# Performance work log

Hardware: AMD Instinct MI355X
Metric: run time of the kernel (lower is better)

The kernel has to match this reference:

```python
import jax, jax.numpy as jnp
import numpy as np

B, T, DIM, HEADS, KPROJ = 4, 4096, 1024, 16, 256
DH = DIM // HEADS  # dim_head = 64


def setup_inputs() -> dict:
    key = jax.random.key(0)
    k1, k2, k3, k4 = jax.random.split(key, 4)
    x = jax.random.normal(k1, (B, T, DIM), dtype=jnp.float32)
    proj_mat = jax.random.normal(k2, (T, KPROJ), dtype=jnp.float32)
    # to_qvk: Linear(dim, 3*dim, bias=False); store as [dim, 3*dim] so y = x @ Wqkv
    Wqkv = jax.random.normal(k3, (DIM, 3 * DIM), dtype=jnp.float32) / np.sqrt(DIM)
    # W_0: Linear(dim, dim, bias=False); stored as [dim, dim] so y = x @ W0
    W0 = jax.random.normal(k4, (DIM, DIM), dtype=jnp.float32) / np.sqrt(DIM)
    return {"x": x, "proj_mat": proj_mat, "Wqkv": Wqkv, "W0": W0}


def reference(x, proj_mat, Wqkv, W0):
    scale = DH ** (-0.5)
    qkv = jnp.einsum('btc,cf->btf', x, Wqkv)  # [B,T,3*dim]
    # einops 'b t (d k h) -> k b h t d' with k=3, h=HEADS: last axis splits as (d, 3, h)
    qkv = qkv.reshape(B, T, DH, 3, HEADS)
    qkv = jnp.transpose(qkv, (3, 0, 4, 1, 2))  # [3, B, H, T, DH]
    q, k, v = qkv[0], qkv[1], qkv[2]
    # Linformer low-rank projection of k and v along sequence axis
    k = jnp.einsum('bhjd,jk->bhkd', k, proj_mat)  # [B,H,KPROJ,DH]
    v = jnp.einsum('bhjd,jk->bhkd', v, proj_mat)
    # scaled dot-product attention
    scores = jnp.einsum('bhid,bhjd->bhij', q, k) * scale  # [B,H,T,KPROJ]
    attn = jax.nn.softmax(scores, axis=-1)
    out = jnp.einsum('bhij,bhjd->bhid', attn, v)  # [B,H,T,DH]
    out = jnp.transpose(out, (0, 2, 1, 3)).reshape(B, T, HEADS * DH)
    return jnp.einsum('btc,cf->btf', out, W0)
```

## Files before the change

kernel.cpp:

```cpp
#include <hip/hip_runtime.h>
#include <stdint.h>
#include <stddef.h>

#define TB    4096
#define NDIM  1024
#define NH    16
#define KPROJ 256
#define DH    64
#define NBH   64

typedef _Float16 f16;
typedef _Float16 f16x8 __attribute__((ext_vector_type(8)));
typedef float    f32x4 __attribute__((ext_vector_type(4)));

__device__ __forceinline__ void glds16(const f16* g, f16* l) {
  __builtin_amdgcn_global_load_lds((const __attribute__((address_space(1))) void*)g,
                                   (__attribute__((address_space(3))) void*)l, 16, 0, 0);
}

__launch_bounds__(256)
__global__ void cvt_x(const float* __restrict__ in, f16* __restrict__ out) {
  size_t i = ((size_t)blockIdx.x * 256 + threadIdx.x) * 8;
  float4 v0 = *(const float4*)(in + i);
  float4 v1 = *(const float4*)(in + i + 4);
  union { f16 h[8]; uint4 u; } pk;
  pk.h[0] = (f16)v0.x; pk.h[1] = (f16)v0.y; pk.h[2] = (f16)v0.z; pk.h[3] = (f16)v0.w;
  pk.h[4] = (f16)v1.x; pk.h[5] = (f16)v1.y; pk.h[6] = (f16)v1.z; pk.h[7] = (f16)v1.w;
  *(uint4*)(out + i) = pk.u;
}

__launch_bounds__(256)
__global__ void cvt_t(const float* __restrict__ in, f16* __restrict__ out, int R, int C) {
  __shared__ __align__(16) f16 s[64][72];
  const int tid = threadIdx.x;
  const int c0 = blockIdx.x * 64, r0 = blockIdx.y * 64;
#pragma unroll
  for (int it = 0; it < 4; ++it) {
    int chunk = it * 256 + tid;
    int r_l = chunk >> 4, c4 = (chunk & 15) * 4;
    float4 v = *(const float4*)(in + (size_t)(r0 + r_l) * C + c0 + c4);
    s[c4 + 0][r_l] = (f16)v.x; s[c4 + 1][r_l] = (f16)v.y;
    s[c4 + 2][r_l] = (f16)v.z; s[c4 + 3][r_l] = (f16)v.w;
  }
  __syncthreads();
#pragma unroll
  for (int it = 0; it < 2; ++it) {
    int chunk = it * 256 + tid;
    int c_l = chunk >> 3, rc = (chunk & 7) * 8;
    *(uint4*)(out + (size_t)(c0 + c_l) * R + r0 + rc) = *(const uint4*)&s[c_l][rc];
  }
}

__launch_bounds__(256)
__global__ void k_q(const f16* __restrict__ Xh, const f16* __restrict__ Wt,
                    f16* __restrict__ qt) {
  __shared__ __align__(16) f16 As[128 * 32];
  __shared__ __align__(16) f16 Bs[128 * 32];
  const int tid = threadIdx.x;
  const int w = tid >> 6, lane = tid & 63;
  const int quad = lane >> 4, l15 = lane & 15;
  const int bn0 = blockIdx.x * 128, bm0 = blockIdx.y * 128;
  const int wm = (w & 1) * 64, wn = (w >> 1) * 64;
  const int srow = lane >> 2, skc = lane & 3;

  f32x4 acc[4][4];
#pragma unroll
  for (int i = 0; i < 4; ++i)
#pragma unroll
    for (int j = 0; j < 4; ++j) acc[i][j] = (f32x4){0.f, 0.f, 0.f, 0.f};

  const f16* Ag0 = Xh + (size_t)(bm0 + w * 32 + srow) * NDIM + skc * 8;
  const int n0 = bn0 + w * 32 + srow, n1 = n0 + 16;
  const f16* Bg0 = Wt + (size_t)(48 * (n0 & 63) + (n0 >> 6)) * NDIM + skc * 8;
  const f16* Bg1 = Wt + (size_t)(48 * (n1 & 63) + (n1 >> 6)) * NDIM + skc * 8;
  f16* Al0 = As + (w * 32) * 32;
  f16* Bl0 = Bs + (w * 32) * 32;

  for (int k0 = 0; k0 < NDIM; k0 += 32) {
    glds16(Ag0 + k0, Al0);
    glds16(Ag0 + (size_t)16 * NDIM + k0, Al0 + 16 * 32);
    glds16(Bg0 + k0, Bl0);
    glds16(Bg1 + k0, Bl0 + 16 * 32);
    __syncthreads();
    f16x8 a[4], bfr[4];
#pragma unroll
    for (int i = 0; i < 4; ++i) a[i] = *(const f16x8*)(As + (wm + i * 16 + l15) * 32 + quad * 8);
#pragma unroll
    for (int j = 0; j < 4; ++j) bfr[j] = *(const f16x8*)(Bs + (wn + j * 16 + l15) * 32 + quad * 8);
#pragma unroll
    for (int i = 0; i < 4; ++i)
#pragma unroll
      for (int j = 0; j < 4; ++j)
        acc[i][j] = __builtin_amdgcn_mfma_f32_16x16x32_f16(a[i], bfr[j], acc[i][j], 0, 0, 0);
    __syncthreads();
  }

#pragma unroll
  for (int i = 0; i < 4; ++i) {
    int mrow = bm0 + wm + i * 16 + quad * 4;
    int bb = mrow >> 12, tt = mrow & 4095;
#pragma unroll
    for (int j = 0; j < 4; ++j) {
      int n = bn0 + wn + j * 16 + l15;
      int h = n >> 6, d = n & 63;
      size_t off = ((size_t)((bb * NH + h) * DH + d)) * TB + tt;
      union { f16 hh[4]; uint2 u; } pk;
#pragma unroll
      for (int r = 0; r < 4; ++r) pk.hh[r] = (f16)acc[i][j][r];
      *(uint2*)(qt + off) = pk.u;
    }
  }
}

__launch_bounds__(256)
__global__ void k_xp(const f16* __restrict__ Pt, const f16* __restrict__ XhT,
                     f16* __restrict__ Xp) {
  __shared__ __align__(16) f16 As[128 * 32];
  __shared__ __align__(16) f16 Bs[64 * 32];
  const int tid = threadIdx.x;
  const int w = tid >> 6, lane = tid & 63;
  const int quad = lane >> 4, l15 = lane & 15;
  const int km0 = blockIdx.x * 128;
  const int c0 = blockIdx.y * 64, b = blockIdx.z;
  const int srow = lane >> 2, skc = lane & 3;
  const f16* Bbase = XhT + ((size_t)b * NDIM + c0) * TB;

  f32x4 acc[2][4];
#pragma unroll
  for (int i = 0; i < 2; ++i)
#pragma unroll
    for (int j = 0; j < 4; ++j) acc[i][j] = (f32x4){0.f, 0.f, 0.f, 0.f};

  const f16* Ag0 = Pt + (size_t)(km0 + w * 32 + srow) * TB + skc * 8;
  const f16* Bg0 = Bbase + (size_t)(w * 16 + srow) * TB + skc * 8;
  f16* Al0 = As + (w * 32) * 32;
  f16* Bl0 = Bs + (w * 16) * 32;

  for (int k0 = 0; k0 < TB; k0 += 32) {
    glds16(Ag0 + k0, Al0);
    glds16(Ag0 + (size_t)16 * TB + k0, Al0 + 16 * 32);
    glds16(Bg0 + k0, Bl0);
    __syncthreads();
    f16x8 a[2], bfr[4];
#pragma unroll
    for (int i = 0; i < 2; ++i) a[i] = *(const f16x8*)(As + (w * 32 + i * 16 + l15) * 32 + quad * 8);
#pragma unroll
    for (int j = 0; j < 4; ++j) bfr[j] = *(const f16x8*)(Bs + (j * 16 + l15) * 32 + quad * 8);
#pragma unroll
    for (int i = 0; i < 2; ++i)
#pragma unroll
      for (int j = 0; j < 4; ++j)
        acc[i][j] = __builtin_amdgcn_mfma_f32_16x16x32_f16(a[i], bfr[j], acc[i][j], 0, 0, 0);
    __syncthreads();
  }

#pragma unroll
  for (int i = 0; i < 2; ++i) {
    int kap0 = km0 + w * 32 + i * 16 + quad * 4;
#pragma unroll
    for (int j = 0; j < 4; ++j) {
      int c = c0 + j * 16 + l15;
#pragma unroll
      for (int r = 0; r < 4; ++r)
        Xp[((size_t)b * KPROJ + kap0 + r) * NDIM + c] = (f16)acc[i][j][r];
    }
  }
}

__launch_bounds__(256)
__global__ void k_kv(const f16* __restrict__ Xp, const f16* __restrict__ Wt,
                     f16* __restrict__ kpv) {
  __shared__ __align__(16) f16 As[128 * 32];
  __shared__ __align__(16) f16 Bs[128 * 32];
  const int tid = threadIdx.x;
  const int w = tid >> 6, lane = tid & 63;
  const int quad = lane >> 4, l15 = lane & 15;
  const int bn0 = blockIdx.x * 128, bm0 = blockIdx.y * 128;
  const int rv = blockIdx.z;
  const int wm = (w & 1) * 64, wn = (w >> 1) * 64;
  const int srow = lane >> 2, skc = lane & 3;

  f32x4 acc[4][4];
#pragma unroll
  for (int i = 0; i < 4; ++i)
#pragma unroll
    for (int j = 0; j < 4; ++j) acc[i][j] = (f32x4){0.f, 0.f, 0.f, 0.f};

  const f16* Ag0 = Xp + (size_t)(bm0 + w * 32 + srow) * NDIM + skc * 8;
  const int n0 = bn0 + w * 32 + srow, n1 = n0 + 16;
  const f16* Bg0 = Wt + (size_t)(48 * (n0 & 63) + 16 * (1 + rv) + (n0 >> 6)) * NDIM + skc * 8;
  const f16* Bg1 = Wt + (size_t)(48 * (n1 & 63) + 16 * (1 + rv) + (n1 >> 6)) * NDIM + skc * 8;
  f16* Al0 = As + (w * 32) * 32;
  f16* Bl0 = Bs + (w * 32) * 32;

  for (int k0 = 0; k0 < NDIM; k0 += 32) {
    glds16(Ag0 + k0, Al0);
    glds16(Ag0 + (size_t)16 * NDIM + k0, Al0 + 16 * 32);
    glds16(Bg0 + k0, Bl0);
    glds16(Bg1 + k0, Bl0 + 16 * 32);
    __syncthreads();
    f16x8 a[4], bfr[4];
#pragma unroll
    for (int i = 0; i < 4; ++i) a[i] = *(const f16x8*)(As + (wm + i * 16 + l15) * 32 + quad * 8);
#pragma unroll
    for (int j = 0; j < 4; ++j) bfr[j] = *(const f16x8*)(Bs + (wn + j * 16 + l15) * 32 + quad * 8);
#pragma unroll
    for (int i = 0; i < 4; ++i)
#pragma unroll
      for (int j = 0; j < 4; ++j)
        acc[i][j] = __builtin_amdgcn_mfma_f32_16x16x32_f16(a[i], bfr[j], acc[i][j], 0, 0, 0);
    __syncthreads();
  }

  if (rv == 0) {
#pragma unroll
    for (int i = 0; i < 4; ++i) {
      int m = bm0 + wm + i * 16 + quad * 4;
      int b = m >> 8, kap = m & 255;
#pragma unroll
      for (int j = 0; j < 4; ++j) {
        int n = bn0 + wn + j * 16 + l15;
        int h = n >> 6, d = n & 63;
#pragma unroll
        for (int r = 0; r < 4; ++r)
          kpv[((size_t)(b * NH + h) * KPROJ + kap + r) * DH + d] = (f16)acc[i][j][r];
      }
    }
  } else {
    f16* vpT = kpv + (size_t)NBH * KPROJ * DH;
#pragma unroll
    for (int i = 0; i < 4; ++i) {
      int m = bm0 + wm + i * 16 + quad * 4;
      int b = m >> 8, kap = m & 255;
#pragma unroll
      for (int j = 0; j < 4; ++j) {
        int n = bn0 + wn + j * 16 + l15;
        int h = n >> 6, d = n & 63;
        union { f16 hh[4]; uint2 u; } pk;
#pragma unroll
        for (int r = 0; r < 4; ++r) pk.hh[r] = (f16)acc[i][j][r];
        *(uint2*)&vpT[((size_t)(b * NH + h) * DH + d) * KPROJ + kap] = pk.u;
      }
    }
  }
}

__launch_bounds__(256)
__global__ void k_attn(const f16* __restrict__ qt, const f16* __restrict__ kpv,
                       f16* __restrict__ aout) {
  __shared__ __align__(16) f16 Ps[4][16][264];
  __shared__ __align__(16) f16 Ks[16384];
  f16* Qs = &Ps[0][0][0];
  const int tid = threadIdx.x;
  const int w = tid >> 6, lane = tid & 63;
  const int quad = lane >> 4, l15 = lane & 15;
  const int bh = blockIdx.y;
  const int tb = blockIdx.x * 64;
  const int b = bh >> 4, h = bh & 15;

  const f16* kpb = kpv + (size_t)bh * (KPROJ * DH);
  const f16* vpb = kpv + (size_t)NBH * KPROJ * DH + (size_t)bh * (DH * KPROJ);

  {
    const f16* qg = qt + (size_t)bh * DH * TB + tb;
#pragma unroll
    for (int c = 0; c < 2; ++c) {
      int d0 = w * 16 + c * 8;
      glds16(qg + (size_t)(d0 + (lane >> 3)) * TB + (lane & 7) * 8, Qs + d0 * 64);
    }
    const int kcolg = ((lane & 7) ^ (lane >> 3)) * 8;
    const int krow0 = w * 64 + (lane >> 3);
#pragma unroll
    for (int it = 0; it < 8; ++it)
      glds16(kpb + (size_t)(krow0 + it * 8) * DH + kcolg, Ks + w * 4096 + it * 512);
  }
  __syncthreads();

  f16x8 aq[2];
#pragma unroll
  for (int ks = 0; ks < 2; ++ks)
#pragma unroll
    for (int j = 0; j < 8; ++j)
      aq[ks][j] = Qs[(ks * 32 + quad * 8 + j) * 64 + w * 16 + l15];

  f32x4 sc[16];
  const int sc0 = (quad ^ (l15 & 7)) * 8;
#pragma unroll
  for (int nt = 0; nt < 16; ++nt) {
    const f16* krow = Ks + (nt * 16 + l15) * 64;
    f16x8 b0 = *(const f16x8*)(krow + sc0);
    f16x8 b1 = *(const f16x8*)(krow + (sc0 ^ 32));
    f32x4 c = (f32x4){0.f, 0.f, 0.f, 0.f};
    c = __builtin_amdgcn_mfma_f32_16x16x32_f16(aq[0], b0, c, 0, 0, 0);
    c = __builtin_amdgcn_mfma_f32_16x16x32_f16(aq[1], b1, c, 0, 0, 0);
    sc[nt] = c;
  }

  float mx[4] = {-1e30f, -1e30f, -1e30f, -1e30f};
#pragma unroll
  for (int nt = 0; nt < 16; ++nt)
#pragma unroll
    for (int r = 0; r < 4; ++r) {
      float s = sc[nt][r] * 0.125f;
      sc[nt][r] = s;
      mx[r] = fmaxf(mx[r], s);
    }
#pragma unroll
  for (int r = 0; r < 4; ++r)
#pragma unroll
    for (int off = 1; off < 16; off <<= 1) mx[r] = fmaxf(mx[r], __shfl_xor(mx[r], off));

  __syncthreads();

  {
#pragma unroll
    for (int it = 0; it < 8; ++it) {
      int r = w * 16 + it * 2 + (lane >> 5);
      int colg = ((lane & 31) ^ (r & 7)) * 8;
      glds16(vpb + (size_t)r * KPROJ + colg, Ks + w * 4096 + it * 512);
    }
  }

  float sm[4] = {0.f, 0.f, 0.f, 0.f};
#pragma unroll
  for (int nt = 0; nt < 16; ++nt)
#pragma unroll
    for (int r = 0; r < 4; ++r) {
      float e = __expf(sc[nt][r] - mx[r]);
      sc[nt][r] = e;
      sm[r] += e;
    }
#pragma unroll
  for (int r = 0; r < 4; ++r)
#pragma unroll
    for (int off = 1; off < 16; off <<= 1) sm[r] += __shfl_xor(sm[r], off);

#pragma unroll
  for (int nt = 0; nt < 16; ++nt)
#pragma unroll
    for (int r = 0; r < 4; ++r) {
      f16 hh = (f16)sc[nt][r];
      uint32_t hb = (uint32_t)__builtin_bit_cast(uint16_t, hh);
      uint32_t nb = (uint32_t)__shfl_xor((int)hb, 1);
      if (!(lane & 1))
        *(uint32_t*)&Ps[w][quad * 4 + r][nt * 16 + l15] = (hb & 0xffffu) | (nb << 16);
    }

  __syncthreads();

  f32x4 oc[4];
#pragma unroll
  for (int j = 0; j < 4; ++j) oc[j] = (f32x4){0.f, 0.f, 0.f, 0.f};
#pragma unroll
  for (int kk = 0; kk < 8; ++kk) {
    f16x8 pa = *(const f16x8*)&Ps[w][l15][kk * 32 + quad * 8];
#pragma unroll
    for (int nd = 0; nd < 4; ++nd) {
      int row = nd * 16 + l15;
      int c = ((kk * 4 + quad) ^ (l15 & 7)) * 8;
      f16x8 bv = *(const f16x8*)(Ks + row * KPROJ + c);
      oc[nd] = __builtin_amdgcn_mfma_f32_16x16x32_f16(pa, bv, oc[nd], 0, 0, 0);
    }
  }

#pragma unroll
  for (int nd = 0; nd < 4; ++nd)
#pragma unroll
    for (int r = 0; r < 4; ++r)
      Ps[w][quad * 4 + r][nd * 16 + l15] = (f16)(oc[nd][r] / sm[r]);

  const int orow = lane >> 3, oc8 = (lane & 7) * 8;
  const size_t obase = ((size_t)b * TB + tb + w * 16) * NDIM + h * 64 + oc8;
#pragma unroll
  for (int g = 0; g < 2; ++g)
    *(f16x8*)(aout + obase + (size_t)(g * 8 + orow) * NDIM) =
        *(const f16x8*)&Ps[w][g * 8 + orow][oc8];
}

__launch_bounds__(256)
__global__ void k_out(const f16* __restrict__ A, const f16* __restrict__ Bt,
                      float* __restrict__ Out) {
  __shared__ __align__(16) f16 As[128 * 32];
  __shared__ __align__(16) f16 Bs[128 * 32];
  const int tid = threadIdx.x;
  const int w = tid >> 6, lane = tid & 63;
  const int quad = lane >> 4, l15 = lane & 15;
  const int bn0 = blockIdx.x * 128, bm0 = blockIdx.y * 128;
  const int wm = (w & 1) * 64, wn = (w >> 1) * 64;
  const int srow = lane >> 2, skc = lane & 3;

  f32x4 acc[4][4];
#pragma unroll
  for (int i = 0; i < 4; ++i)
#pragma unroll
    for (int j = 0; j < 4; ++j) acc[i][j] = (f32x4){0.f, 0.f, 0.f, 0.f};

  const f16* Ag0 = A + (size_t)(bm0 + w * 32 + srow) * NDIM + skc * 8;
  const f16* Bg0 = Bt + (size_t)(bn0 + w * 32 + srow) * NDIM + skc * 8;
  f16* Al0 = As + (w * 32) * 32;
  f16* Bl0 = Bs + (w * 32) * 32;

  for (int k0 = 0; k0 < NDIM; k0 += 32) {
    glds16(Ag0 + k0, Al0);
    glds16(Ag0 + (size_t)16 * NDIM + k0, Al0 + 16 * 32);
    glds16(Bg0 + k0, Bl0);
    glds16(Bg0 + (size_t)16 * NDIM + k0, Bl0 + 16 * 32);
    __syncthreads();
    f16x8 a[4], b[4];
#pragma unroll
    for (int i = 0; i < 4; ++i) a[i] = *(const f16x8*)(As + (wm + i * 16 + l15) * 32 + quad * 8);
#pragma unroll
    for (int j = 0; j < 4; ++j) b[j] = *(const f16x8*)(Bs + (wn + j * 16 + l15) * 32 + quad * 8);
#pragma unroll
    for (int i = 0; i < 4; ++i)
#pragma unroll
      for (int j = 0; j < 4; ++j)
        acc[i][j] = __builtin_amdgcn_mfma_f32_16x16x32_f16(a[i], b[j], acc[i][j], 0, 0, 0);
    __syncthreads();
  }

#pragma unroll
  for (int i = 0; i < 4; ++i) {
    int m = bm0 + wm + i * 16 + quad * 4;
#pragma unroll
    for (int j = 0; j < 4; ++j) {
      int n = bn0 + wn + j * 16 + l15;
#pragma unroll
      for (int r = 0; r < 4; ++r) Out[(size_t)(m + r) * NDIM + n] = acc[i][j][r];
    }
  }
}

extern "C" void kernel_launch(void* const* d_in, const int* in_sizes, int n_in,
                              void* d_out, int out_size, void* d_ws, size_t ws_size,
                              hipStream_t stream) {
  const float* X    = (const float*)d_in[0];
  const float* P    = (const float*)d_in[1];
  const float* Wqkv = (const float*)d_in[2];
  const float* W0   = (const float*)d_in[3];
  float* Out = (float*)d_out;

  char* ws = (char*)d_ws;
  const size_t MB = 1ull << 20;
  f16* Xh   = (f16*)(ws);
  f16* aout = (f16*)(ws);
  f16* qt   = (f16*)(ws + 32 * MB);
  f16* XhT  = (f16*)(ws + 64 * MB);
  f16* Xp   = (f16*)(ws + 96 * MB);
  f16* kpv  = (f16*)(ws + 128 * MB);
  f16* Wqt  = (f16*)(ws + 132 * MB);
  f16* W0t  = (f16*)(ws + 138 * MB);
  f16* Ptb  = (f16*)(ws + 140 * MB);

  cvt_x<<<dim3(8192), 256, 0, stream>>>(X, Xh);
  cvt_t<<<dim3(48, 16), 256, 0, stream>>>(Wqkv, Wqt, 1024, 3072);
  cvt_t<<<dim3(16, 16), 256, 0, stream>>>(W0, W0t, 1024, 1024);
  cvt_t<<<dim3(4, 64), 256, 0, stream>>>(P, Ptb, 4096, 256);
  for (int b = 0; b < 4; ++b)
    cvt_t<<<dim3(16, 64), 256, 0, stream>>>(X + (size_t)b * 4194304,
                                            XhT + (size_t)b * 4194304, 4096, 1024);
  k_q<<<dim3(8, 128), 256, 0, stream>>>(Xh, Wqt, qt);
  k_xp<<<dim3(2, 16, 4), 256, 0, stream>>>(Ptb, XhT, Xp);
  k_kv<<<dim3(8, 8, 2), 256, 0, stream>>>(Xp, Wqt, kpv);
  k_attn<<<dim3(64, 64), 256, 0, stream>>>(qt, kpv, aout);
  k_out<<<dim3(8, 128), 256, 0, stream>>>(aout, W0t, Out);
}
```

Baseline: 416.5 us.

## Fuse x conversion passes, fold softmax scale into Q, double attention rows per block

Merges the linear fp16 conversion of x with the transposed conversion so x is read from global memory once instead of twice. The 1/sqrt(dh) scale is applied in the Q projection epilogue rather than in the attention kernel. The attention kernel now handles 128 query rows per block in two groups, reusing the loaded K and V tiles, and replaces division by a reciprocal multiply. The trade-off is higher register pressure (launch bounds now request 2 waves per SIMD) and half as many attention blocks.

```diff
diff --git a/kernel.cpp b/kernel.cpp
--- a/kernel.cpp
+++ b/kernel.cpp
@@ -19,14 +19,29 @@
 }
 
 __launch_bounds__(256)
-__global__ void cvt_x(const float* __restrict__ in, f16* __restrict__ out) {
-  size_t i = ((size_t)blockIdx.x * 256 + threadIdx.x) * 8;
-  float4 v0 = *(const float4*)(in + i);
-  float4 v1 = *(const float4*)(in + i + 4);
-  union { f16 h[8]; uint4 u; } pk;
-  pk.h[0] = (f16)v0.x; pk.h[1] = (f16)v0.y; pk.h[2] = (f16)v0.z; pk.h[3] = (f16)v0.w;
-  pk.h[4] = (f16)v1.x; pk.h[5] = (f16)v1.y; pk.h[6] = (f16)v1.z; pk.h[7] = (f16)v1.w;
-  *(uint4*)(out + i) = pk.u;
+__global__ void cvt_xt(const float* __restrict__ in, f16* __restrict__ out_lin,
+                       f16* __restrict__ out_t, int R, int C) {
+  __shared__ __align__(16) f16 s[64][72];
+  const int tid = threadIdx.x;
+  const int c0 = blockIdx.x * 64, r0 = blockIdx.y * 64;
+#pragma unroll
+  for (int it = 0; it < 4; ++it) {
+    int chunk = it * 256 + tid;
+    int r_l = chunk >> 4, c4 = (chunk & 15) * 4;
+    float4 v = *(const float4*)(in + (size_t)(r0 + r_l) * C + c0 + c4);
+    union { f16 h[4]; uint2 u; } pk;
+    pk.h[0] = (f16)v.x; pk.h[1] = (f16)v.y; pk.h[2] = (f16)v.z; pk.h[3] = (f16)v.w;
+    *(uint2*)(out_lin + (size_t)(r0 + r_l) * C + c0 + c4) = pk.u;
+    s[c4 + 0][r_l] = pk.h[0]; s[c4 + 1][r_l] = pk.h[1];
+    s[c4 + 2][r_l] = pk.h[2]; s[c4 + 3][r_l] = pk.h[3];
+  }
+  __syncthreads();
+#pragma unroll
+  for (int it = 0; it < 2; ++it) {
+    int chunk = it * 256 + tid;
+    int c_l = chunk >> 3, rc = (chunk & 7) * 8;
+    *(uint4*)(out_t + (size_t)(c0 + c_l) * R + r0 + rc) = *(const uint4*)&s[c_l][rc];
+  }
 }
 
 __launch_bounds__(256)
@@ -106,7 +121,7 @@
       size_t off = ((size_t)((bb * NH + h) * DH + d)) * TB + tt;
       union { f16 hh[4]; uint2 u; } pk;
 #pragma unroll
-      for (int r = 0; r < 4; ++r) pk.hh[r] = (f16)acc[i][j][r];
+      for (int r = 0; r < 4; ++r) pk.hh[r] = (f16)(acc[i][j][r] * 0.125f);
       *(uint2*)(qt + off) = pk.u;
     }
   }
@@ -245,7 +260,7 @@
   }
 }
 
-__launch_bounds__(256)
+__launch_bounds__(256, 2)
 __global__ void k_attn(const f16* __restrict__ qt, const f16* __restrict__ kpv,
                        f16* __restrict__ aout) {
   __shared__ __align__(16) f16 Ps[4][16][264];
@@ -255,7 +270,7 @@
   const int w = tid >> 6, lane = tid & 63;
   const int quad = lane >> 4, l15 = lane & 15;
   const int bh = blockIdx.y;
-  const int tb = blockIdx.x * 64;
+  const int tb = blockIdx.x * 128;
   const int b = bh >> 4, h = bh & 15;
 
   const f16* kpb = kpv + (size_t)bh * (KPROJ * DH);
@@ -264,9 +279,9 @@
   {
     const f16* qg = qt + (size_t)bh * DH * TB + tb;
 #pragma unroll
-    for (int c = 0; c < 2; ++c) {
-      int d0 = w * 16 + c * 8;
-      glds16(qg + (size_t)(d0 + (lane >> 3)) * TB + (lane & 7) * 8, Qs + d0 * 64);
+    for (int c = 0; c < 4; ++c) {
+      int d0 = w * 16 + c * 4;
+      glds16(qg + (size_t)(d0 + (lane >> 4)) * TB + (lane & 15) * 8, Qs + d0 * 128);
     }
     const int kcolg = ((lane & 7) ^ (lane >> 3)) * 8;
     const int krow0 = w * 64 + (lane >> 3);
@@ -276,39 +291,47 @@
   }
   __syncthreads();
 
-  f16x8 aq[2];
-#pragma unroll
-  for (int ks = 0; ks < 2; ++ks)
-#pragma unroll
-    for (int j = 0; j < 8; ++j)
-      aq[ks][j] = Qs[(ks * 32 + quad * 8 + j) * 64 + w * 16 + l15];
-
-  f32x4 sc[16];
+  f16x8 aq[2][2];
+#pragma unroll
+  for (int g = 0; g < 2; ++g)
+#pragma unroll
+    for (int ks = 0; ks < 2; ++ks)
+#pragma unroll
+      for (int j = 0; j < 8; ++j)
+        aq[g][ks][j] = Qs[(ks * 32 + quad * 8 + j) * 128 + g * 64 + w * 16 + l15];
+
+  f32x4 sc[2][16];
   const int sc0 = (quad ^ (l15 & 7)) * 8;
 #pragma unroll
-  for (int nt = 0; nt < 16; ++nt) {
-    const f16* krow = Ks + (nt * 16 + l15) * 64;
-    f16x8 b0 = *(const f16x8*)(krow + sc0);
-    f16x8 b1 = *(const f16x8*)(krow + (sc0 ^ 32));
-    f32x4 c = (f32x4){0.f, 0.f, 0.f, 0.f};
-    c = __builtin_amdgcn_mfma_f32_16x16x32_f16(aq[0], b0, c, 0, 0, 0);
-    c = __builtin_amdgcn_mfma_f32_16x16x32_f16(aq[1], b1, c, 0, 0, 0);
-    sc[nt] = c;
-  }
-
-  float mx[4] = {-1e30f, -1e30f, -1e30f, -1e30f};
-#pragma unroll
-  for (int nt = 0; nt < 16; ++nt)
-#pragma unroll
-    for (int r = 0; r < 4; ++r) {
-      float s = sc[nt][r] * 0.125f;
-      sc[nt][r] = s;
-      mx[r] = fmaxf(mx[r], s);
-    }
-#pragma unroll
-  for (int r = 0; r < 4; ++r)
-#pragma unroll
-    for (int off = 1; off < 16; off <<= 1) mx[r] = fmaxf(mx[r], __shfl_xor(mx[r], off));
+  for (int g = 0; g < 2; ++g)
+#pragma unroll
+    for (int nt = 0; nt < 16; ++nt) {
+      const f16* krow = Ks + (nt * 16 + l15) * 64;
+      f16x8 b0 = *(const f16x8*)(krow + sc0);
+      f16x8 b1 = *(const f16x8*)(krow + (sc0 ^ 32));
+      f32x4 c = (f32x4){0.f, 0.f, 0.f, 0.f};
+      c = __builtin_amdgcn_mfma_f32_16x16x32_f16(aq[g][0], b0, c, 0, 0, 0);
+      c = __builtin_amdgcn_mfma_f32_16x16x32_f16(aq[g][1], b1, c, 0, 0, 0);
+      sc[g][nt] = c;
+    }
+
+  float mx[2][4];
+#pragma unroll
+  for (int g = 0; g < 2; ++g)
+#pragma unroll
+    for (int r = 0; r < 4; ++r) mx[g][r] = -1e30f;
+#pragma unroll
+  for (int g = 0; g < 2; ++g)
+#pragma unroll
+    for (int nt = 0; nt < 16; ++nt)
+#pragma unroll
+      for (int r = 0; r < 4; ++r) mx[g][r] = fmaxf(mx[g][r], sc[g][nt][r]);
+#pragma unroll
+  for (int g = 0; g < 2; ++g)
+#pragma unroll
+    for (int r = 0; r < 4; ++r)
+#pragma unroll
+      for (int off = 1; off < 16; off <<= 1) mx[g][r] = fmaxf(mx[g][r], __shfl_xor(mx[g][r], off));
 
   __syncthreads();
 
@@ -321,25 +344,34 @@
     }
   }
 
-  float sm[4] = {0.f, 0.f, 0.f, 0.f};
+  float sm[2][4] = {{0.f, 0.f, 0.f, 0.f}, {0.f, 0.f, 0.f, 0.f}};
+#pragma unroll
+  for (int g = 0; g < 2; ++g)
+#pragma unroll
+    for (int nt = 0; nt < 16; ++nt)
+#pragma unroll
+      for (int r = 0; r < 4; ++r) {
+        float e = __expf(sc[g][nt][r] - mx[g][r]);
+        sc[g][nt][r] = e;
+        sm[g][r] += e;
+      }
+#pragma unroll
+  for (int g = 0; g < 2; ++g)
+#pragma unroll
+    for (int r = 0; r < 4; ++r)
+#pragma unroll
+      for (int off = 1; off < 16; off <<= 1) sm[g][r] += __shfl_xor(sm[g][r], off);
+  float rs[2][4];
+#pragma unroll
+  for (int g = 0; g < 2; ++g)
+#pragma unroll
+    for (int r = 0; r < 4; ++r) rs[g][r] = 1.0f / sm[g][r];
+
 #pragma unroll
   for (int nt = 0; nt < 16; ++nt)
 #pragma unroll
     for (int r = 0; r < 4; ++r) {
-      float e = __expf(sc[nt][r] - mx[r]);
-      sc[nt][r] = e;
-      sm[r] += e;
-    }
-#pragma unroll
-  for (int r = 0; r < 4; ++r)
-#pragma unroll
-    for (int off = 1; off < 16; off <<= 1) sm[r] += __shfl_xor(sm[r], off);
-
-#pragma unroll
-  for (int nt = 0; nt < 16; ++nt)
-#pragma unroll
-    for (int r = 0; r < 4; ++r) {
-      f16 hh = (f16)sc[nt][r];
+      f16 hh = (f16)sc[0][nt][r];
       uint32_t hb = (uint32_t)__builtin_bit_cast(uint16_t, hh);
       uint32_t nb = (uint32_t)__shfl_xor((int)hb, 1);
       if (!(lane & 1))
@@ -348,33 +380,50 @@
 
   __syncthreads();
 
-  f32x4 oc[4];
-#pragma unroll
-  for (int j = 0; j < 4; ++j) oc[j] = (f32x4){0.f, 0.f, 0.f, 0.f};
-#pragma unroll
-  for (int kk = 0; kk < 8; ++kk) {
-    f16x8 pa = *(const f16x8*)&Ps[w][l15][kk * 32 + quad * 8];
-#pragma unroll
-    for (int nd = 0; nd < 4; ++nd) {
-      int row = nd * 16 + l15;
-      int c = ((kk * 4 + quad) ^ (l15 & 7)) * 8;
-      f16x8 bv = *(const f16x8*)(Ks + row * KPROJ + c);
-      oc[nd] = __builtin_amdgcn_mfma_f32_16x16x32_f16(pa, bv, oc[nd], 0, 0, 0);
-    }
-  }
-
-#pragma unroll
-  for (int nd = 0; nd < 4; ++nd)
-#pragma unroll
-    for (int r = 0; r < 4; ++r)
-      Ps[w][quad * 4 + r][nd * 16 + l15] = (f16)(oc[nd][r] / sm[r]);
-
   const int orow = lane >> 3, oc8 = (lane & 7) * 8;
-  const size_t obase = ((size_t)b * TB + tb + w * 16) * NDIM + h * 64 + oc8;
-#pragma unroll
-  for (int g = 0; g < 2; ++g)
-    *(f16x8*)(aout + obase + (size_t)(g * 8 + orow) * NDIM) =
-        *(const f16x8*)&Ps[w][g * 8 + orow][oc8];
+
+#pragma unroll
+  for (int g = 0; g < 2; ++g) {
+    if (g == 1) {
+#pragma unroll
+      for (int nt = 0; nt < 16; ++nt)
+#pragma unroll
+        for (int r = 0; r < 4; ++r) {
+          f16 hh = (f16)sc[1][nt][r];
+          uint32_t hb = (uint32_t)__builtin_bit_cast(uint16_t, hh);
+          uint32_t nb = (uint32_t)__shfl_xor((int)hb, 1);
+          if (!(lane & 1))
+            *(uint32_t*)&Ps[w][quad * 4 + r][nt * 16 + l15] = (hb & 0xffffu) | (nb << 16);
+        }
+    }
+
+    f32x4 oc[4];
+#pragma unroll
+    for (int j = 0; j < 4; ++j) oc[j] = (f32x4){0.f, 0.f, 0.f, 0.f};
+#pragma unroll
+    for (int kk = 0; kk < 8; ++kk) {
+      f16x8 pa = *(const f16x8*)&Ps[w][l15][kk * 32 + quad * 8];
+#pragma unroll
+      for (int nd = 0; nd < 4; ++nd) {
+        int row = nd * 16 + l15;
+        int c = ((kk * 4 + quad) ^ (l15 & 7)) * 8;
+        f16x8 bv = *(const f16x8*)(Ks + row * KPROJ + c);
+        oc[nd] = __builtin_amdgcn_mfma_f32_16x16x32_f16(pa, bv, oc[nd], 0, 0, 0);
+      }
+    }
+
+#pragma unroll
+    for (int nd = 0; nd < 4; ++nd)
+#pragma unroll
+      for (int r = 0; r < 4; ++r)
+        Ps[w][quad * 4 + r][nd * 16 + l15] = (f16)(oc[nd][r] * rs[g][r]);
+
+    const size_t obase = ((size_t)b * TB + tb + g * 64 + w * 16) * NDIM + h * 64 + oc8;
+#pragma unroll
+    for (int gg = 0; gg < 2; ++gg)
+      *(f16x8*)(aout + obase + (size_t)(gg * 8 + orow) * NDIM) =
+          *(const f16x8*)&Ps[w][gg * 8 + orow][oc8];
+  }
 }
 
 __launch_bounds__(256)
@@ -452,16 +501,16 @@
   f16* W0t  = (f16*)(ws + 138 * MB);
   f16* Ptb  = (f16*)(ws + 140 * MB);
 
-  cvt_x<<<dim3(8192), 256, 0, stream>>>(X, Xh);
+  for (int b = 0; b < 4; ++b)
+    cvt_xt<<<dim3(16, 64), 256, 0, stream>>>(X + (size_t)b * 4194304,
+                                             Xh + (size_t)b * 4194304,
+                                             XhT + (size_t)b * 4194304, 4096, 1024);
   cvt_t<<<dim3(48, 16), 256, 0, stream>>>(Wqkv, Wqt, 1024, 3072);
   cvt_t<<<dim3(16, 16), 256, 0, stream>>>(W0, W0t, 1024, 1024);
   cvt_t<<<dim3(4, 64), 256, 0, stream>>>(P, Ptb, 4096, 256);
-  for (int b = 0; b < 4; ++b)
-    cvt_t<<<dim3(16, 64), 256, 0, stream>>>(X + (size_t)b * 4194304,
-                                            XhT + (size_t)b * 4194304, 4096, 1024);
   k_q<<<dim3(8, 128), 256, 0, stream>>>(Xh, Wqt, qt);
   k_xp<<<dim3(2, 16, 4), 256, 0, stream>>>(Ptb, XhT, Xp);
   k_kv<<<dim3(8, 8, 2), 256, 0, stream>>>(Xp, Wqt, kpv);
-  k_attn<<<dim3(64, 64), 256, 0, stream>>>(qt, kpv, aout);
+  k_attn<<<dim3(32, 64), 256, 0, stream>>>(qt, kpv, aout);
   k_out<<<dim3(8, 128), 256, 0, stream>>>(aout, W0t, Out);
 }
```

Result: faster. 404.2 us (-2.9%).
